# Kernel optimization log

Measured on AMD Instinct MI355X. Metric: run time of the kernel, lower is better.

Reference implementation:

```python
import jax, jax.numpy as jnp
import numpy as np

B, T = 2, 512
D, H, DFF = 1024, 16, 4096
V, CSL = 32000, 16
NL, NDL = 4, 2
MAXLEN = 1024
DH = D // H


def generate_ar_mask(L, csl):
    m = np.zeros((2 * L, 2 * L), dtype=bool)
    for i in range(L):
        m[:i] = True
        m[L + (i // csl) * csl: L + i] = True
    return jnp.asarray(m)


def generate_block_ntp_mask(L, csl):
    m = np.zeros((2 * L, 2 * L), dtype=bool)
    for c in range(L // csl):
        if c - 1 >= 0:
            m[:(c - 1) * csl] = True
        m[L + c * csl: L + (c + 1) * csl] = True
    return jnp.asarray(m)


def layernorm(x, g, b, eps=1e-5):
    mu = x.mean(-1, keepdims=True)
    var = x.var(-1, keepdims=True)
    return (x - mu) / jnp.sqrt(var + eps) * g + b


def block(x, mask, p):
    ln1g, ln1b, wqkv, bqkv, wo, bo, ln2g, ln2b, w1, b1, w2, b2 = p
    h = layernorm(x, ln1g, ln1b)
    qkv = h @ wqkv + bqkv                       # [B,S,3D]
    q, k, v = jnp.split(qkv, 3, axis=-1)
    bs, S, _ = x.shape
    q = q.reshape(bs, S, H, DH).transpose(0, 2, 1, 3)
    k = k.reshape(bs, S, H, DH).transpose(0, 2, 1, 3)
    v = v.reshape(bs, S, H, DH).transpose(0, 2, 1, 3)
    scores = jnp.einsum('bhqd,bhkd->bhqk', q, k) / jnp.sqrt(jnp.asarray(DH, x.dtype))
    scores = jnp.where(mask, scores, jnp.asarray(-1e9, x.dtype))
    attn = jax.nn.softmax(scores, axis=-1)
    o = jnp.einsum('bhqk,bhkd->bhqd', attn, v)
    o = o.transpose(0, 2, 1, 3).reshape(bs, S, D)
    x = x + (o @ wo + bo)
    h = layernorm(x, ln2g, ln2b)
    return x + (jax.nn.gelu(h @ w1 + b1, approximate=False) @ w2 + b2)


def setup_inputs():
    key = jax.random.key(0)
    ks = jax.random.split(key, 6)

    def pstack(k, n):
        kk = jax.random.split(k, 4)
        return dict(
            ln1g=jnp.ones((n, D)), ln1b=jnp.zeros((n, D)),
            wqkv=0.02 * jax.random.normal(kk[0], (n, D, 3 * D)), bqkv=jnp.zeros((n, 3 * D)),
            wo=0.02 * jax.random.normal(kk[1], (n, D, D)), bo=jnp.zeros((n, D)),
            ln2g=jnp.ones((n, D)), ln2b=jnp.zeros((n, D)),
            w1=0.02 * jax.random.normal(kk[2], (n, D, DFF)), b1=jnp.zeros((n, DFF)),
            w2=0.02 * jax.random.normal(kk[3], (n, DFF, D)), b2=jnp.zeros((n, D)))

    body = pstack(ks[0], NL)
    dec = pstack(ks[1], NDL)
    inp = {
        'tok_ids': jax.random.randint(ks[2], (B, T), 0, V),
        'tok_emb': 0.02 * jax.random.normal(ks[3], (V, D)),
        'pos_emb': 0.02 * jax.random.normal(ks[4], (MAXLEN, D)),
        'mask_tokens': 0.02 * jax.random.normal(ks[5], (1, CSL, D)),
    }
    for kname, vv in body.items():
        inp['b_' + kname] = vv
    for kname, vv in dec.items():
        inp['d_' + kname] = vv
    return inp


def reference(tok_ids, tok_emb, pos_emb, mask_tokens,
              b_ln1g, b_ln1b, b_wqkv, b_bqkv, b_wo, b_bo, b_ln2g, b_ln2b, b_w1, b_b1, b_w2, b_b2,
              d_ln1g, d_ln1b, d_wqkv, d_bqkv, d_wo, d_bo, d_ln2g, d_ln2b, d_w1, d_b1, d_w2, d_b2):
    Bq, Tq = tok_ids.shape
    pos = jnp.tile(jnp.arange(Tq), 2)            # pos ids repeated for both halves
    emb_pos = pos_emb[pos]                       # [2T, D], broadcast over batch
    mask_ids = jnp.tile(mask_tokens, (Bq, Tq // CSL, 1))
    x = jnp.concatenate([tok_emb[tok_ids], mask_ids], axis=1) + emb_pos[None]

    body_mask = generate_block_ntp_mask(Tq, CSL)
    bp = (b_ln1g, b_ln1b, b_wqkv, b_bqkv, b_wo, b_bo, b_ln2g, b_ln2b, b_w1, b_b1, b_w2, b_b2)
    for i in range(NL):
        x = block(x, body_mask, tuple(p[i] for p in bp))

    ar_mask = generate_ar_mask(Tq, CSL)
    dp = (d_ln1g, d_ln1b, d_wqkv, d_bqkv, d_wo, d_bo, d_ln2g, d_ln2b, d_w1, d_b1, d_w2, d_b2)
    for i in range(NDL):
        x = block(x, ar_mask, tuple(p[i] for p in dp))

    logits = (x @ tok_emb.T)[:, Tq + 1:, :]      # [B, T-1, V]
    tgt = tok_ids[:, :-1].reshape(-1)
    logits = logits.reshape(-1, V)
    logp = jax.nn.log_softmax(logits, axis=-1)
    loss = -jnp.take_along_axis(logp, tgt[:, None], axis=1).mean()
    return loss
```

## Files before the change

### kernel.cpp

```cpp
#include <hip/hip_runtime.h>
#include <hip/hip_bf16.h>
#include <math.h>

#define DD   1024
#define HHN  16
#define DHD  64
#define DFFN 4096
#define VV   32000
#define BBN  2
#define TTN  512
#define SSN  1024
#define NRN  2048

typedef __attribute__((ext_vector_type(8))) short short8;
typedef __attribute__((ext_vector_type(4))) float f32x4;

enum : long {
    LSTR    = 12582912,
    OFF_QKV = 0,
    OFF_WO  = 3145728,
    OFF_W1  = 4194304,
    OFF_W2  = 8388608
};

struct P24 { const float* p[24]; };

__device__ __forceinline__ unsigned short f2bf(float f) {
    __hip_bfloat16 h = __float2bfloat16(f);
    return __builtin_bit_cast(unsigned short, h);
}
__device__ __forceinline__ float bf2f(unsigned short u) {
    return __bfloat162float(__builtin_bit_cast(__hip_bfloat16, u));
}

__device__ __forceinline__ void glds16(const void* g, void* l) {
    __builtin_amdgcn_global_load_lds(
        (const __attribute__((address_space(1))) void*)g,
        (__attribute__((address_space(3))) void*)l,
        16, 0, 0);
}

__device__ __forceinline__ float blockReduceSum(float v) {
    __shared__ float sh[4];
    #pragma unroll
    for (int o = 1; o < 64; o <<= 1) v += __shfl_xor(v, o, 64);
    int lane = threadIdx.x & 63, wv = threadIdx.x >> 6;
    __syncthreads();
    if (lane == 0) sh[wv] = v;
    __syncthreads();
    return sh[0] + sh[1] + sh[2] + sh[3];
}

__global__ __launch_bounds__(256) void prep_k(P24 wp, unsigned short* __restrict__ wbf,
                                              const int* __restrict__ tok,
                                              const float* __restrict__ temb,
                                              const float* __restrict__ pemb,
                                              const float* __restrict__ mtok,
                                              float* __restrict__ x) {
    __shared__ __align__(16) unsigned short Lb[128 * 72];
    const int id = blockIdx.x;
    const int t = threadIdx.x;

    if (id < 9216) {
        int seg, base, K, N;
        long woff;
        if (id < 2304)      { seg = 0; base = 0;    K = DD;   N = 3 * DD; woff = OFF_QKV; }
        else if (id < 3072) { seg = 1; base = 2304; K = DD;   N = DD;     woff = OFF_WO;  }
        else if (id < 6144) { seg = 2; base = 3072; K = DD;   N = DFFN;   woff = OFF_W1;  }
        else                { seg = 3; base = 6144; K = DFFN; N = DD;     woff = OFF_W2;  }
        const int rid = id - base;
        const int tpl = (K / 128) * (N / 64);
        const int lz = rid / tpl, t2 = rid % tpl;
        const int nt = N / 64;
        const int n0 = (t2 % nt) * 64, k0 = (t2 / nt) * 128;
        const float* w = wp.p[seg * 6 + lz];
        unsigned short* wt = wbf + (size_t)lz * LSTR + woff;

        const int kr = t >> 4;
        const int nc = (t & 15) * 4;
        #pragma unroll
        for (int p = 0; p < 8; p++) {
            const int k = p * 16 + kr;
            const int g = ((k >> 6) & 1) << 4;
            float4 f = *(const float4*)(w + (size_t)(k0 + k) * N + n0 + nc);
            __align__(8) unsigned short tmp[4];
            tmp[0] = f2bf(f.x); tmp[1] = f2bf(f.y);
            tmp[2] = f2bf(f.z); tmp[3] = f2bf(f.w);
            *(unsigned long long*)&Lb[k * 72 + (nc ^ g)] =
                *(const unsigned long long*)tmp;
        }
        __syncthreads();
        {
            const int rp  = t >> 3;
            const int sub = t & 7;
            const int kcg = sub >> 2;
            const int kh  = sub & 3;
            const int colx = (2 * rp) ^ (kcg << 4);
            const int kb = kcg * 64 + kh * 16;
            __align__(16) unsigned short tA[16], tB[16];
            #pragma unroll
            for (int i = 0; i < 16; i++) {
                unsigned int v = *(const unsigned int*)&Lb[(kb + i) * 72 + colx];
                tA[i] = (unsigned short)(v & 0xffff);
                tB[i] = (unsigned short)(v >> 16);
            }
            unsigned short* d0 = wt + (size_t)(n0 + 2 * rp) * K + k0 + kb;
            unsigned short* d1 = d0 + K;
            #pragma unroll
            for (int i = 0; i < 2; i++) {
                ((int4*)d0)[i] = ((const int4*)tA)[i];
                ((int4*)d1)[i] = ((const int4*)tB)[i];
            }
        }
    } else {
        const int row = id - 9216;
        const int b = row >> 10, s = row & 1023;
        const int d = t * 4;
        const float* src;
        const float* pe;
        if (s < TTN) {
            int tid2 = tok[b * TTN + s];
            src = temb + (size_t)tid2 * DD + d;
            pe  = pemb + (size_t)s * DD + d;
        } else {
            int sm = s - TTN;
            src = mtok + (size_t)(sm & 15) * DD + d;
            pe  = pemb + (size_t)sm * DD + d;
        }
        float4 v = *(const float4*)src;
        float4 p = *(const float4*)pe;
        v.x += p.x; v.y += p.y; v.z += p.z; v.w += p.w;
        *(float4*)(x + (size_t)row * DD + d) = v;
    }
}

__global__ __launch_bounds__(256) void ln_k(const float* __restrict__ x,
                                            const float* __restrict__ g,
                                            const float* __restrict__ b,
                                            unsigned short* __restrict__ out) {
    int row = blockIdx.x;
    int d = threadIdx.x * 4;
    const float4 v = *(const float4*)(x + (size_t)row * DD + d);
    float s  = v.x + v.y + v.z + v.w;
    float ss = v.x * v.x + v.y * v.y + v.z * v.z + v.w * v.w;
    s  = blockReduceSum(s);
    ss = blockReduceSum(ss);
    float mu  = s * (1.0f / DD);
    float var = ss * (1.0f / DD) - mu * mu;
    float inv = rsqrtf(var + 1e-5f);
    const float4 gg = *(const float4*)(g + d);
    const float4 bb = *(const float4*)(b + d);
    ushort4 o;
    o.x = f2bf((v.x - mu) * inv * gg.x + bb.x);
    o.y = f2bf((v.y - mu) * inv * gg.y + bb.y);
    o.z = f2bf((v.z - mu) * inv * gg.z + bb.z);
    o.w = f2bf((v.w - mu) * inv * gg.w + bb.w);
    *(ushort4*)(out + (size_t)row * DD + d) = o;
}

__global__ __launch_bounds__(256, 4) void flash_k(
    const unsigned short* __restrict__ qkvb,
    unsigned short* __restrict__ o,
    int mtype) {
    __shared__ __align__(16) unsigned short Qs[64][72];
    __shared__ __align__(16) unsigned short Ks[64][72];
    __shared__ __align__(16) unsigned short Vs[64][72];
    __shared__ __align__(16) unsigned short Ps[64][72];
    __shared__ float vcol[64];

    const int blk = blockIdx.x;
    const int bh = blk >> 4, qt = blk & 15;
    const int b = bh >> 4, h = bh & 15;
    const int t = threadIdx.x;
    const int lane = t & 63;
    const int w = t >> 6;
    const int fr = lane & 15;
    const int g8 = (lane >> 4) * 8;
    const int g4 = (lane >> 4) * 4;

    {
        const int r = t >> 2, c0 = (t & 3) * 16;
        const unsigned short* src =
            qkvb + (size_t)(b * SSN + qt * 64 + r) * 3072 + h * 64 + c0;
        *(int4*)&Qs[r][c0]     = *(const int4*)(src);
        *(int4*)&Qs[r][c0 + 8] = *(const int4*)(src + 8);
    }
    __syncthreads();
    short8 aq[2];
    #pragma unroll
    for (int kk = 0; kk < 2; kk++)
        aq[kk] = *(const short8*)&Qs[w * 16 + fr][kk * 32 + g8];

    float rsum[4] = {0.f, 0.f, 0.f, 0.f};
    f32x4 accO[4] = {};

    float vacc[16];
    #pragma unroll
    for (int j = 0; j < 16; j++) vacc[j] = 0.f;

    const unsigned short* kbase = qkvb + (size_t)(b * SSN) * 3072 + DD + h * 64;
    const unsigned short* vbase = qkvb + (size_t)(b * SSN) * 3072 + 2 * DD + h * 64;
    const int d0 = w * 16;

    for (int kt = 0; kt < 16; kt++) {
        __syncthreads();
        {
            const int r = t >> 2, c0 = (t & 3) * 16;
            const unsigned short* src = kbase + (size_t)(kt * 64 + r) * 3072 + c0;
            *(int4*)&Ks[r][c0]     = *(const int4*)(src);
            *(int4*)&Ks[r][c0 + 8] = *(const int4*)(src + 8);
        }
        {
            const unsigned short* src = vbase + (size_t)(kt * 64 + lane) * 3072 + d0;
            int4 q0 = *(const int4*)(src);
            int4 q1 = *(const int4*)(src + 8);
            const unsigned short* u = (const unsigned short*)&q0;
            #pragma unroll
            for (int j = 0; j < 8; j++) {
                Vs[d0 + j][lane] = u[j];
                vacc[j] += bf2f(u[j]);
            }
            const unsigned short* u2 = (const unsigned short*)&q1;
            #pragma unroll
            for (int j = 0; j < 8; j++) {
                Vs[d0 + 8 + j][lane] = u2[j];
                vacc[8 + j] += bf2f(u2[j]);
            }
        }
        __syncthreads();

        f32x4 a2[4] = {};
        #pragma unroll
        for (int n = 0; n < 4; n++) {
            short8 bk0 = *(const short8*)&Ks[n * 16 + fr][g8];
            short8 bk1 = *(const short8*)&Ks[n * 16 + fr][32 + g8];
            a2[n] = __builtin_amdgcn_mfma_f32_16x16x32_bf16(aq[0], bk0, a2[n], 0, 0, 0);
            a2[n] = __builtin_amdgcn_mfma_f32_16x16x32_bf16(aq[1], bk1, a2[n], 0, 0, 0);
        }
        #pragma unroll
        for (int j = 0; j < 4; j++) {
            #pragma unroll
            for (int n = 0; n < 4; n++) {
                float pv = __expf(a2[n][j] * 0.125f);
                rsum[j] += pv;
                Ps[w * 16 + g4 + j][n * 16 + fr] = f2bf(pv);
            }
        }
        #pragma unroll
        for (int kk = 0; kk < 2; kk++) {
            short8 pa = *(const short8*)&Ps[w * 16 + fr][kk * 32 + g8];
            #pragma unroll
            for (int nd = 0; nd < 4; nd++) {
                short8 vb = *(const short8*)&Vs[nd * 16 + fr][kk * 32 + g8];
                accO[nd] = __builtin_amdgcn_mfma_f32_16x16x32_bf16(pa, vb, accO[nd], 0, 0, 0);
            }
        }
    }

    float lrun[4];
    #pragma unroll
    for (int j = 0; j < 4; j++) {
        float rs = rsum[j];
        #pragma unroll
        for (int o2 = 1; o2 < 16; o2 <<= 1) rs += __shfl_xor(rs, o2, 64);
        lrun[j] = rs;
    }

    #pragma unroll
    for (int j = 0; j < 16; j++) {
        float vs = vacc[j];
        #pragma unroll
        for (int o2 = 1; o2 < 64; o2 <<= 1) vs += __shfl_xor(vs, o2, 64);
        if (lane == j) vcol[d0 + j] = vs;
    }
    __syncthreads();

    #pragma unroll
    for (int nd = 0; nd < 4; nd++)
        #pragma unroll
        for (int j = 0; j < 4; j++) {
            const int row = qt * 64 + w * 16 + g4 + j;
            const int col = nd * 16 + fr;
            bool uni;
            if (mtype == 0) uni = (row >= 480 && row < 512);
            else            uni = (row == 511) || (row >= 512 && (row & 15) == 15);
            float val;
            if (uni) val = vcol[col] * (1.0f / 1024.0f);
            else     val = accO[nd][j] / lrun[j];
            o[(size_t)(b * SSN + row) * DD + h * 64 + col] = f2bf(val);
        }
}

__global__ __launch_bounds__(256) void gxlconv_k(const float* __restrict__ x,
                                                 unsigned short* __restrict__ xl,
                                                 const float* __restrict__ temb,
                                                 unsigned short* __restrict__ tembb) {
    const int id = blockIdx.x;
    const int t = threadIdx.x;
    if (id < 1024) {
        int d = t * 4;
        ushort4 o = {0, 0, 0, 0};
        if (id < 1022) {
            int b = id / 511, i = id % 511;
            float4 v = *(const float4*)(x + (size_t)(b * SSN + 513 + i) * DD + d);
            o.x = f2bf(v.x); o.y = f2bf(v.y); o.z = f2bf(v.z); o.w = f2bf(v.w);
        }
        *(ushort4*)(xl + (size_t)id * DD + d) = o;
    } else {
        long i = ((long)(id - 1024) * 256 + t) * 8;
        float4 a = *(const float4*)(temb + i);
        float4 b = *(const float4*)(temb + i + 4);
        __align__(16) unsigned short tmp[8];
        tmp[0] = f2bf(a.x); tmp[1] = f2bf(a.y); tmp[2] = f2bf(a.z); tmp[3] = f2bf(a.w);
        tmp[4] = f2bf(b.x); tmp[5] = f2bf(b.y); tmp[6] = f2bf(b.z); tmp[7] = f2bf(b.w);
        *(int4*)(tembb + i) = *(const int4*)tmp;
    }
}

__global__ __launch_bounds__(256) void loss_row2_k(const float2* __restrict__ part,
                                                   const float* __restrict__ tgtlog,
                                                   float* __restrict__ out) {
    const int r = blockIdx.x;
    const int t = threadIdx.x;
    float mx = -1e30f, s = 0.f;
    if (t < 250) {
        float2 p = part[(size_t)r * 250 + t];
        mx = p.x; s = p.y;
    }
    #pragma unroll
    for (int o2 = 1; o2 < 64; o2 <<= 1) {
        float om = __shfl_xor(mx, o2, 64);
        float os = __shfl_xor(s, o2, 64);
        float m2 = fmaxf(mx, om);
        s = s * __expf(mx - m2) + os * __expf(om - m2);
        mx = m2;
    }
    __shared__ float shm[4], shs[4];
    int lane = t & 63, wv = t >> 6;
    if (lane == 0) { shm[wv] = mx; shs[wv] = s; }
    __syncthreads();
    if (t == 0) {
        float M = fmaxf(fmaxf(shm[0], shm[1]), fmaxf(shm[2], shm[3]));
        float S = shs[0] * __expf(shm[0] - M) + shs[1] * __expf(shm[1] - M)
                + shs[2] * __expf(shm[2] - M) + shs[3] * __expf(shm[3] - M);
        atomicAdd(out, ((logf(S) + M) - tgtlog[r]) * (1.0f / 1022.0f));
    }
}

template <int EPI, int KSPLIT, int BM>
__global__ __launch_bounds__(256) void gemm_k(
    const unsigned short* __restrict__ A, long lda,
    const unsigned short* __restrict__ Bt, long ldb,
    void* __restrict__ Cp, long ldc,
    const float* __restrict__ bias,
    int MT, int K, long kstr) {
    constexpr int MFRAG = BM / 32;
    __shared__ __align__(16) unsigned short As[2][BM][32];
    __shared__ __align__(16) unsigned short Bs[2][128][32];

    const int nwg = gridDim.x;
    const int q = nwg >> 3, r = nwg & 7;
    const int xcd = blockIdx.x & 7, lin = blockIdx.x >> 3;
    const int wg = (xcd < r ? xcd * (q + 1) : r * (q + 1) + (xcd - r) * q) + lin;
    const int tiles = nwg / KSPLIT;
    const int ks = wg / tiles;
    const int rem = wg % tiles;
    const int brow = (rem % MT) * BM;
    const int bcol = (rem / MT) * 128;
    const int Kl = K / KSPLIT;

    const int t = threadIdx.x;
    const int lane = t & 63;
    const int w = t >> 6;
    const int fr = lane & 15;
    const int g8 = (lane >> 4) * 8;

    const int sc = (lane & 3) * 8;
    const int srB = w * 32 + (lane >> 2);
    const unsigned short* bP0 = Bt + (size_t)(bcol + srB) * ldb + ks * Kl + sc;
    const unsigned short* bP1 = bP0 + (size_t)16 * ldb;
    const int srA = (BM == 128 ? w * 32 : w * 16) + (lane >> 2);
    const unsigned short* aP0 = A + (size_t)(brow + srA) * lda + ks * Kl + sc;
    const unsigned short* aP1 = aP0 + (size_t)16 * lda;

    f32x4 acc[MFRAG][4] = {};
    const int nsteps = Kl >> 5;

    auto stage = [&](int buf) {
        if constexpr (BM == 128) {
            glds16(aP0, &As[buf][w * 32][0]);
            glds16(aP1, &As[buf][w * 32 + 16][0]);
        } else {
            glds16(aP0, &As[buf][w * 16][0]);
        }
        glds16(bP0, &Bs[buf][w * 32][0]);
        glds16(bP1, &Bs[buf][w * 32 + 16][0]);
        aP0 += 32; aP1 += 32; bP0 += 32; bP1 += 32;
    };

    stage(0);
    asm volatile("s_waitcnt vmcnt(0)");
    __syncthreads();

    const int wrB = (w >> 1) * (BM / 2);
    int cur = 0;
    for (int s2 = 1; s2 < nsteps; ++s2) {
        const int nb = cur ^ 1;
        stage(nb);

        short8 af[MFRAG], bf[4];
        #pragma unroll
        for (int m = 0; m < MFRAG; m++)
            af[m] = *(const short8*)&As[cur][wrB + m * 16 + fr][g8];
        #pragma unroll
        for (int n = 0; n < 4; n++)
            bf[n] = *(const short8*)&Bs[cur][(w & 1) * 64 + n * 16 + fr][g8];
        #pragma unroll
        for (int m = 0; m < MFRAG; m++)
            #pragma unroll
            for (int n = 0; n < 4; n++)
                acc[m][n] = __builtin_amdgcn_mfma_f32_16x16x32_bf16(af[m], bf[n], acc[m][n], 0, 0, 0);
        __syncthreads();
        cur = nb;
    }
    {
        short8 af[MFRAG], bf[4];
        #pragma unroll
        for (int m = 0; m < MFRAG; m++)
            af[m] = *(const short8*)&As[cur][wrB + m * 16 + fr][g8];
        #pragma unroll
        for (int n = 0; n < 4; n++)
            bf[n] = *(const short8*)&Bs[cur][(w & 1) * 64 + n * 16 + fr][g8];
        #pragma unroll
        for (int m = 0; m < MFRAG; m++)
            #pragma unroll
            for (int n = 0; n < 4; n++)
                acc[m][n] = __builtin_amdgcn_mfma_f32_16x16x32_bf16(af[m], bf[n], acc[m][n], 0, 0, 0);
    }

    const int wc = (w & 1) * 64;
    const int g4 = (lane >> 4) * 4;
    #pragma unroll
    for (int n = 0; n < 4; n++) {
        const int col = bcol + wc + n * 16 + fr;
        const float bv = (bias && (KSPLIT == 1 || ks == 0)) ? bias[col] : 0.f;
        #pragma unroll
        for (int m = 0; m < MFRAG; m++) {
            #pragma unroll
            for (int j = 0; j < 4; j++) {
                const int row = brow + wrB + m * 16 + g4 + j;
                float v = acc[m][n][j] + bv;
                const size_t ci = (size_t)row * ldc + col;
                if (EPI == 0) {
                    ((float*)Cp)[ci] = v;
                } else if (EPI == 1) {
                    ((unsigned short*)Cp)[ci] = f2bf(v);
                } else if (EPI == 2) {
                    float gl = 0.5f * v * (1.0f + erff(v * 0.70710678118654752f));
                    ((unsigned short*)Cp)[ci] = f2bf(gl);
                } else if (EPI == 3) {
                    ((float*)Cp)[ci] += v;
                } else {
                    atomicAdd(&((float*)Cp)[ci], v);
                }
            }
        }
    }
}

__global__ __launch_bounds__(256, 1) void gemm_lse_k(
    const unsigned short* __restrict__ A,
    const unsigned short* __restrict__ Bt,
    float2* __restrict__ part,
    float* __restrict__ tgtlog,
    const int* __restrict__ tok) {
    __shared__ __align__(16) unsigned short As[2][128][32];
    __shared__ __align__(16) unsigned short Bs[2][256][32];

    const int nwg = gridDim.x;
    const int q = nwg >> 3, r = nwg & 7;
    const int xcd = blockIdx.x & 7, lin = blockIdx.x >> 3;
    const int wg = (xcd < r ? xcd * (q + 1) : r * (q + 1) + (xcd - r) * q) + lin;
    const int MT = 8;
    const int brow = (wg % MT) * 128;
    const int bcol = (wg / MT) * 256;

    const int t = threadIdx.x;
    const int lane = t & 63;
    const int w = t >> 6;
    const int fr = lane & 15;
    const int g8 = (lane >> 4) * 8;

    const int sc = (lane & 3) * 8;
    const int srA = w * 32 + (lane >> 2);
    const unsigned short* aP0 = A + (size_t)(brow + srA) * DD + sc;
    const unsigned short* aP1 = aP0 + (size_t)16 * DD;
    const int srB = w * 64 + (lane >> 2);
    const unsigned short* bP0 = Bt + (size_t)(bcol + srB) * DD + sc;
    const unsigned short* bP1 = bP0 + (size_t)16 * DD;
    const unsigned short* bP2 = bP0 + (size_t)32 * DD;
    const unsigned short* bP3 = bP0 + (size_t)48 * DD;

    f32x4 acc[4][8] = {};

    auto stage = [&](int buf) {
        glds16(aP0, &As[buf][w * 32][0]);
        glds16(aP1, &As[buf][w * 32 + 16][0]);
        glds16(bP0, &Bs[buf][w * 64][0]);
        glds16(bP1, &Bs[buf][w * 64 + 16][0]);
        glds16(bP2, &Bs[buf][w * 64 + 32][0]);
        glds16(bP3, &Bs[buf][w * 64 + 48][0]);
        aP0 += 32; aP1 += 32;
        bP0 += 32; bP1 += 32; bP2 += 32; bP3 += 32;
    };

    stage(0);
    asm volatile("s_waitcnt vmcnt(0)");
    __syncthreads();

    int cur = 0;
    for (int s2 = 1; s2 < 32; ++s2) {
        const int nb = cur ^ 1;
        stage(nb);

        short8 af[4], bf[8];
        #pragma unroll
        for (int m = 0; m < 4; m++)
            af[m] = *(const short8*)&As[cur][(w >> 1) * 64 + m * 16 + fr][g8];
        #pragma unroll
        for (int n = 0; n < 8; n++)
            bf[n] = *(const short8*)&Bs[cur][(w & 1) * 128 + n * 16 + fr][g8];
        #pragma unroll
        for (int m = 0; m < 4; m++)
            #pragma unroll
            for (int n = 0; n < 8; n++)
                acc[m][n] = __builtin_amdgcn_mfma_f32_16x16x32_bf16(af[m], bf[n], acc[m][n], 0, 0, 0);
        __syncthreads();
        cur = nb;
    }
    {
        short8 af[4], bf[8];
        #pragma unroll
        for (int m = 0; m < 4; m++)
            af[m] = *(const short8*)&As[cur][(w >> 1) * 64 + m * 16 + fr][g8];
        #pragma unroll
        for (int n = 0; n < 8; n++)
            bf[n] = *(const short8*)&Bs[cur][(w & 1) * 128 + n * 16 + fr][g8];
        #pragma unroll
        for (int m = 0; m < 4; m++)
            #pragma unroll
            for (int n = 0; n < 8; n++)
                acc[m][n] = __builtin_amdgcn_mfma_f32_16x16x32_bf16(af[m], bf[n], acc[m][n], 0, 0, 0);
    }

    const int wr = (w >> 1) * 64;
    const int wc = (w & 1) * 128;
    const int g4 = (lane >> 4) * 4;
    const int ct2 = (bcol >> 7) + (w & 1);
    #pragma unroll
    for (int m = 0; m < 4; m++) {
        #pragma unroll
        for (int j = 0; j < 4; j++) {
            const int grow = brow + wr + m * 16 + g4 + j;
            float vv[8];
            #pragma unroll
            for (int n = 0; n < 8; n++) vv[n] = acc[m][n][j];
            float mx = vv[0];
            #pragma unroll
            for (int n = 1; n < 8; n++) mx = fmaxf(mx, vv[n]);
            #pragma unroll
            for (int o2 = 1; o2 < 16; o2 <<= 1) mx = fmaxf(mx, __shfl_xor(mx, o2, 64));
            float s = 0.f;
            #pragma unroll
            for (int n = 0; n < 8; n++) s += __expf(vv[n] - mx);
            #pragma unroll
            for (int o2 = 1; o2 < 16; o2 <<= 1) s += __shfl_xor(s, o2, 64);
            if (fr == 0) {
                float2 p; p.x = mx; p.y = s;
                part[(size_t)grow * 250 + ct2] = p;
            }
            int tgtc = -1;
            if (grow < 511) tgtc = tok[grow];
            else if (grow >= 511 && grow < 1022) tgtc = tok[512 + grow - 511];
            const int cl = tgtc - (bcol + wc);
            if (tgtc >= 0 && cl >= 0 && cl < 128 && (cl & 15) == fr) {
                tgtlog[grow] = vv[cl >> 4];
            }
        }
    }
}

extern "C" void kernel_launch(void* const* d_in, const int* in_sizes, int n_in,
                              void* d_out, int out_size, void* d_ws, size_t ws_size,
                              hipStream_t stream) {
    const int*   tok  = (const int*)d_in[0];
    const float* temb = (const float*)d_in[1];
    const float* pemb = (const float*)d_in[2];
    const float* mtok = (const float*)d_in[3];
    const float* W[24];
    for (int i = 0; i < 24; i++) W[i] = (const float*)d_in[4 + i];

    char* ws = (char*)d_ws;
    float*          x      = (float*)(ws + 0);
    unsigned short* xb     = (unsigned short*)(ws + 8388608);
    unsigned short* qkvb   = (unsigned short*)(ws + 12582912);
    unsigned short* o      = (unsigned short*)(ws + 25165824);
    unsigned short* g      = (unsigned short*)(ws + 29360128);
    unsigned short* wbf    = (unsigned short*)(ws + 79691776);
    unsigned short* tembb  = (unsigned short*)(ws + 79691776);
    float2*         part   = (float2*)(ws + 145227776);
    float*          tgtlog = (float*)(ws + 147275776);
    unsigned short* xl     = (unsigned short*)(ws + 230686720);
    float*          rowloss= (float*)(ws + 232783872);
    (void)rowloss;

    P24 wp;
    for (int l = 0; l < 6; l++) {
        const int grp = (l < 4) ? 0 : 1;
        const int li  = (l < 4) ? l : l - 4;
        const float* const* P = W + grp * 12;
        wp.p[0 + l]  = P[2]  + (size_t)li * DD * 3 * DD;
        wp.p[6 + l]  = P[4]  + (size_t)li * DD * DD;
        wp.p[12 + l] = P[8]  + (size_t)li * DD * DFFN;
        wp.p[18 + l] = P[10] + (size_t)li * DFFN * DD;
    }
    hipMemsetAsync(d_out, 0, 4, stream);
    prep_k<<<9216 + 2048, 256, 0, stream>>>(wp, wbf, tok, temb, pemb, mtok, x);

    for (int l = 0; l < 6; l++) {
        const int grp = (l < 4) ? 0 : 1;
        const int li  = (l < 4) ? l : l - 4;
        const float* const* P = W + grp * 12;
        const float* ln1g = P[0] + (size_t)li * DD;
        const float* ln1b = P[1] + (size_t)li * DD;
        const float* bqkv = P[3] + (size_t)li * 3 * DD;
        const float* bo   = P[5] + (size_t)li * DD;
        const float* ln2g = P[6] + (size_t)li * DD;
        const float* ln2b = P[7] + (size_t)li * DD;
        const float* b1   = P[9] + (size_t)li * DFFN;
        const float* b2   = P[11] + (size_t)li * DD;
        unsigned short* wl = wbf + (size_t)l * LSTR;

        if (l == 0) ln_k<<<NRN, 256, 0, stream>>>(x, ln1g, ln1b, xb);
        gemm_k<1, 1, 64><<<32 * 24, 256, 0, stream>>>(xb, DD, wl + OFF_QKV, DD,
                                                      qkvb, 3 * DD, bqkv, 32, DD, 0);
        flash_k<<<512, 256, 0, stream>>>(qkvb, o, grp);
        gemm_k<3, 1, 64><<<32 * 8, 256, 0, stream>>>(o, DD, wl + OFF_WO, DD,
                                                     x, DD, bo, 32, DD, 0);

        ln_k<<<NRN, 256, 0, stream>>>(x, ln2g, ln2b, xb);
        gemm_k<2, 1, 128><<<16 * 32, 256, 0, stream>>>(xb, DD, wl + OFF_W1, DD,
                                                       g, DFFN, b1, 16, DD, 0);
        gemm_k<4, 4, 128><<<16 * 8 * 4, 256, 0, stream>>>(g, DFFN, wl + OFF_W2, DFFN,
                                                          x, DD, b2, 16, DFFN, 0);
        if (l < 5) {
            const int l2 = l + 1;
            const int grp2 = (l2 < 4) ? 0 : 1;
            const int li2  = (l2 < 4) ? l2 : l2 - 4;
            const float* const* P2 = W + grp2 * 12;
            ln_k<<<NRN, 256, 0, stream>>>(x, P2[0] + (size_t)li2 * DD,
                                          P2[1] + (size_t)li2 * DD, xb);
        } else {
            gxlconv_k<<<1024 + 16000, 256, 0, stream>>>(x, xl, temb, tembb);
        }
    }

    gemm_lse_k<<<1000, 256, 0, stream>>>(xl, tembb, part, tgtlog, tok);
    loss_row2_k<<<1022, 256, 0, stream>>>(part, tgtlog, (float*)d_out);
}
```

Measured before the change: 1.414 ms.

## Fuse layernorms into GEMM epilogues via last-block counters; merge embedding conversions into prep

```diff
diff --git a/kernel.cpp b/kernel.cpp
--- a/kernel.cpp
+++ b/kernel.cpp
@@ -51,12 +51,51 @@
     return sh[0] + sh[1] + sh[2] + sh[3];
 }
 
+__device__ __forceinline__ void dev_ln_row(const float* __restrict__ x,
+                                           const float* __restrict__ g,
+                                           const float* __restrict__ b,
+                                           unsigned short* __restrict__ out, int row) {
+    const int lane = threadIdx.x & 63;
+    float4 v[4];
+    float s = 0.f, ss = 0.f;
+    #pragma unroll
+    for (int c = 0; c < 4; c++) {
+        v[c] = *(const float4*)(x + (size_t)row * DD + c * 256 + lane * 4);
+        s  += v[c].x + v[c].y + v[c].z + v[c].w;
+        ss += v[c].x * v[c].x + v[c].y * v[c].y + v[c].z * v[c].z + v[c].w * v[c].w;
+    }
+    #pragma unroll
+    for (int o2 = 1; o2 < 64; o2 <<= 1) {
+        s  += __shfl_xor(s, o2, 64);
+        ss += __shfl_xor(ss, o2, 64);
+    }
+    const float mu  = s * (1.0f / DD);
+    const float var = ss * (1.0f / DD) - mu * mu;
+    const float inv = rsqrtf(var + 1e-5f);
+    #pragma unroll
+    for (int c = 0; c < 4; c++) {
+        const int d = c * 256 + lane * 4;
+        const float4 gg = *(const float4*)(g + d);
+        const float4 bb = *(const float4*)(b + d);
+        ushort4 ov;
+        ov.x = f2bf((v[c].x - mu) * inv * gg.x + bb.x);
+        ov.y = f2bf((v[c].y - mu) * inv * gg.y + bb.y);
+        ov.z = f2bf((v[c].z - mu) * inv * gg.z + bb.z);
+        ov.w = f2bf((v[c].w - mu) * inv * gg.w + bb.w);
+        *(ushort4*)(out + (size_t)row * DD + d) = ov;
+    }
+}
+
 __global__ __launch_bounds__(256) void prep_k(P24 wp, unsigned short* __restrict__ wbf,
                                               const int* __restrict__ tok,
                                               const float* __restrict__ temb,
                                               const float* __restrict__ pemb,
                                               const float* __restrict__ mtok,
-                                              float* __restrict__ x) {
+                                              float* __restrict__ x,
+                                              const float* __restrict__ ln0g,
+                                              const float* __restrict__ ln0b,
+                                              unsigned short* __restrict__ xb,
+                                              unsigned short* __restrict__ tembb) {
     __shared__ __align__(16) unsigned short Lb[128 * 72];
     const int id = blockIdx.x;
     const int t = threadIdx.x;
@@ -112,7 +151,7 @@
                 ((int4*)d1)[i] = ((const int4*)tB)[i];
             }
         }
-    } else {
+    } else if (id < 11264) {
         const int row = id - 9216;
         const int b = row >> 10, s = row & 1023;
         const int d = t * 4;
@@ -131,31 +170,30 @@
         float4 p = *(const float4*)pe;
         v.x += p.x; v.y += p.y; v.z += p.z; v.w += p.w;
         *(float4*)(x + (size_t)row * DD + d) = v;
-    }
-}
-
-__global__ __launch_bounds__(256) void ln_k(const float* __restrict__ x,
-                                            const float* __restrict__ g,
-                                            const float* __restrict__ b,
-                                            unsigned short* __restrict__ out) {
-    int row = blockIdx.x;
-    int d = threadIdx.x * 4;
-    const float4 v = *(const float4*)(x + (size_t)row * DD + d);
-    float s  = v.x + v.y + v.z + v.w;
-    float ss = v.x * v.x + v.y * v.y + v.z * v.z + v.w * v.w;
-    s  = blockReduceSum(s);
-    ss = blockReduceSum(ss);
-    float mu  = s * (1.0f / DD);
-    float var = ss * (1.0f / DD) - mu * mu;
-    float inv = rsqrtf(var + 1e-5f);
-    const float4 gg = *(const float4*)(g + d);
-    const float4 bb = *(const float4*)(b + d);
-    ushort4 o;
-    o.x = f2bf((v.x - mu) * inv * gg.x + bb.x);
-    o.y = f2bf((v.y - mu) * inv * gg.y + bb.y);
-    o.z = f2bf((v.z - mu) * inv * gg.z + bb.z);
-    o.w = f2bf((v.w - mu) * inv * gg.w + bb.w);
-    *(ushort4*)(out + (size_t)row * DD + d) = o;
+        float su  = v.x + v.y + v.z + v.w;
+        float ssu = v.x * v.x + v.y * v.y + v.z * v.z + v.w * v.w;
+        su  = blockReduceSum(su);
+        ssu = blockReduceSum(ssu);
+        const float mu  = su * (1.0f / DD);
+        const float var = ssu * (1.0f / DD) - mu * mu;
+        const float inv = rsqrtf(var + 1e-5f);
+        const float4 gg = *(const float4*)(ln0g + d);
+        const float4 bb = *(const float4*)(ln0b + d);
+        ushort4 ov;
+        ov.x = f2bf((v.x - mu) * inv * gg.x + bb.x);
+        ov.y = f2bf((v.y - mu) * inv * gg.y + bb.y);
+        ov.z = f2bf((v.z - mu) * inv * gg.z + bb.z);
+        ov.w = f2bf((v.w - mu) * inv * gg.w + bb.w);
+        *(ushort4*)(xb + (size_t)row * DD + d) = ov;
+    } else {
+        long i = ((long)(id - 11264) * 256 + t) * 8;
+        float4 a = *(const float4*)(temb + i);
+        float4 b = *(const float4*)(temb + i + 4);
+        __align__(16) unsigned short tmp[8];
+        tmp[0] = f2bf(a.x); tmp[1] = f2bf(a.y); tmp[2] = f2bf(a.z); tmp[3] = f2bf(a.w);
+        tmp[4] = f2bf(b.x); tmp[5] = f2bf(b.y); tmp[6] = f2bf(b.z); tmp[7] = f2bf(b.w);
+        *(int4*)(tembb + i) = *(const int4*)tmp;
+    }
 }
 
 __global__ __launch_bounds__(256, 4) void flash_k(
@@ -265,7 +303,6 @@
         for (int o2 = 1; o2 < 16; o2 <<= 1) rs += __shfl_xor(rs, o2, 64);
         lrun[j] = rs;
     }
-
     #pragma unroll
     for (int j = 0; j < 16; j++) {
         float vs = vacc[j];
@@ -291,32 +328,6 @@
         }
 }
 
-__global__ __launch_bounds__(256) void gxlconv_k(const float* __restrict__ x,
-                                                 unsigned short* __restrict__ xl,
-                                                 const float* __restrict__ temb,
-                                                 unsigned short* __restrict__ tembb) {
-    const int id = blockIdx.x;
-    const int t = threadIdx.x;
-    if (id < 1024) {
-        int d = t * 4;
-        ushort4 o = {0, 0, 0, 0};
-        if (id < 1022) {
-            int b = id / 511, i = id % 511;
-            float4 v = *(const float4*)(x + (size_t)(b * SSN + 513 + i) * DD + d);
-            o.x = f2bf(v.x); o.y = f2bf(v.y); o.z = f2bf(v.z); o.w = f2bf(v.w);
-        }
-        *(ushort4*)(xl + (size_t)id * DD + d) = o;
-    } else {
-        long i = ((long)(id - 1024) * 256 + t) * 8;
-        float4 a = *(const float4*)(temb + i);
-        float4 b = *(const float4*)(temb + i + 4);
-        __align__(16) unsigned short tmp[8];
-        tmp[0] = f2bf(a.x); tmp[1] = f2bf(a.y); tmp[2] = f2bf(a.z); tmp[3] = f2bf(a.w);
-        tmp[4] = f2bf(b.x); tmp[5] = f2bf(b.y); tmp[6] = f2bf(b.z); tmp[7] = f2bf(b.w);
-        *(int4*)(tembb + i) = *(const int4*)tmp;
-    }
-}
-
 __global__ __launch_bounds__(256) void loss_row2_k(const float2* __restrict__ part,
                                                    const float* __restrict__ tgtlog,
                                                    float* __restrict__ out) {
@@ -353,10 +364,13 @@
     const unsigned short* __restrict__ Bt, long ldb,
     void* __restrict__ Cp, long ldc,
     const float* __restrict__ bias,
-    int MT, int K, long kstr) {
+    int MT, int K,
+    const float* __restrict__ lng, const float* __restrict__ lnb,
+    unsigned short* __restrict__ xbo, unsigned* __restrict__ cnt) {
     constexpr int MFRAG = BM / 32;
     __shared__ __align__(16) unsigned short As[2][BM][32];
     __shared__ __align__(16) unsigned short Bs[2][128][32];
+    __shared__ int lastf;
 
     const int nwg = gridDim.x;
     const int q = nwg >> 3, r = nwg & 7;
@@ -451,17 +465,49 @@
                 const int row = brow + wrB + m * 16 + g4 + j;
                 float v = acc[m][n][j] + bv;
                 const size_t ci = (size_t)row * ldc + col;
-                if (EPI == 0) {
-                    ((float*)Cp)[ci] = v;
-                } else if (EPI == 1) {
+                if (EPI == 1) {
                     ((unsigned short*)Cp)[ci] = f2bf(v);
                 } else if (EPI == 2) {
                     float gl = 0.5f * v * (1.0f + erff(v * 0.70710678118654752f));
                     ((unsigned short*)Cp)[ci] = f2bf(gl);
-                } else if (EPI == 3) {
+                } else if (EPI == 3 || EPI == 5) {
                     ((float*)Cp)[ci] += v;
                 } else {
                     atomicAdd(&((float*)Cp)[ci], v);
+                }
+            }
+        }
+    }
+
+    if constexpr (EPI == 5 || EPI == 6) {
+        __syncthreads();
+        if (t == 0) {
+            __threadfence();
+            unsigned old = __hip_atomic_fetch_add(cnt + (rem % MT), 1u,
+                                                  __ATOMIC_ACQ_REL,
+                                                  __HIP_MEMORY_SCOPE_AGENT);
+            lastf = (old == (unsigned)(nwg / MT - 1));
+        }
+        __syncthreads();
+        if (lastf) {
+            __threadfence();
+            const float* xsrc = (const float*)Cp;
+            if (lng) {
+                for (int rr = w; rr < BM; rr += 4)
+                    dev_ln_row(xsrc, lng, lnb, xbo, brow + rr);
+            } else {
+                const int d = t * 4;
+                for (int rr = 0; rr < BM; ++rr) {
+                    const int row = brow + rr;
+                    const int s = row & 1023;
+                    if (s >= 513) {
+                        const int xr = (row >> 10) * 511 + (s - 513);
+                        float4 v = *(const float4*)(xsrc + (size_t)row * DD + d);
+                        ushort4 ov;
+                        ov.x = f2bf(v.x); ov.y = f2bf(v.y);
+                        ov.z = f2bf(v.z); ov.w = f2bf(v.w);
+                        *(ushort4*)(xbo + (size_t)xr * DD + d) = ov;
+                    }
                 }
             }
         }
@@ -607,12 +653,11 @@
     unsigned short* o      = (unsigned short*)(ws + 25165824);
     unsigned short* g      = (unsigned short*)(ws + 29360128);
     unsigned short* wbf    = (unsigned short*)(ws + 79691776);
-    unsigned short* tembb  = (unsigned short*)(ws + 79691776);
-    float2*         part   = (float2*)(ws + 145227776);
-    float*          tgtlog = (float*)(ws + 147275776);
-    unsigned short* xl     = (unsigned short*)(ws + 230686720);
-    float*          rowloss= (float*)(ws + 232783872);
-    (void)rowloss;
+    unsigned short* tembb  = (unsigned short*)(ws + 230686720);
+    float2*         part   = (float2*)(ws + 296222720);
+    float*          tgtlog = (float*)(ws + 298270720);
+    unsigned short* xl     = (unsigned short*)(ws + 298274816);
+    unsigned*       cnt    = (unsigned*)(ws + 300371968);
 
     P24 wp;
     for (int l = 0; l < 6; l++) {
@@ -624,15 +669,17 @@
         wp.p[12 + l] = P[8]  + (size_t)li * DD * DFFN;
         wp.p[18 + l] = P[10] + (size_t)li * DFFN * DD;
     }
+
+    hipMemsetAsync(cnt, 0, 2048, stream);
     hipMemsetAsync(d_out, 0, 4, stream);
-    prep_k<<<9216 + 2048, 256, 0, stream>>>(wp, wbf, tok, temb, pemb, mtok, x);
+
+    prep_k<<<9216 + 2048 + 16000, 256, 0, stream>>>(wp, wbf, tok, temb, pemb, mtok, x,
+                                                    W[0], W[1], xb, tembb);
 
     for (int l = 0; l < 6; l++) {
         const int grp = (l < 4) ? 0 : 1;
         const int li  = (l < 4) ? l : l - 4;
         const float* const* P = W + grp * 12;
-        const float* ln1g = P[0] + (size_t)li * DD;
-        const float* ln1b = P[1] + (size_t)li * DD;
         const float* bqkv = P[3] + (size_t)li * 3 * DD;
         const float* bo   = P[5] + (size_t)li * DD;
         const float* ln2g = P[6] + (size_t)li * DD;
@@ -640,29 +687,36 @@
         const float* b1   = P[9] + (size_t)li * DFFN;
         const float* b2   = P[11] + (size_t)li * DD;
         unsigned short* wl = wbf + (size_t)l * LSTR;
-
-        if (l == 0) ln_k<<<NRN, 256, 0, stream>>>(x, ln1g, ln1b, xb);
-        gemm_k<1, 1, 64><<<32 * 24, 256, 0, stream>>>(xb, DD, wl + OFF_QKV, DD,
-                                                      qkvb, 3 * DD, bqkv, 32, DD, 0);
-        flash_k<<<512, 256, 0, stream>>>(qkvb, o, grp);
-        gemm_k<3, 1, 64><<<32 * 8, 256, 0, stream>>>(o, DD, wl + OFF_WO, DD,
-                                                     x, DD, bo, 32, DD, 0);
-
-        ln_k<<<NRN, 256, 0, stream>>>(x, ln2g, ln2b, xb);
-        gemm_k<2, 1, 128><<<16 * 32, 256, 0, stream>>>(xb, DD, wl + OFF_W1, DD,
-                                                       g, DFFN, b1, 16, DD, 0);
-        gemm_k<4, 4, 128><<<16 * 8 * 4, 256, 0, stream>>>(g, DFFN, wl + OFF_W2, DFFN,
-                                                          x, DD, b2, 16, DFFN, 0);
+        unsigned* cntWo = cnt + l * 64;
+        unsigned* cntF2 = cnt + l * 64 + 32;
+
+        const float* nx_g = nullptr;
+        const float* nx_b = nullptr;
+        unsigned short* f2out = xl;
         if (l < 5) {
             const int l2 = l + 1;
             const int grp2 = (l2 < 4) ? 0 : 1;
             const int li2  = (l2 < 4) ? l2 : l2 - 4;
             const float* const* P2 = W + grp2 * 12;
-            ln_k<<<NRN, 256, 0, stream>>>(x, P2[0] + (size_t)li2 * DD,
-                                          P2[1] + (size_t)li2 * DD, xb);
-        } else {
-            gxlconv_k<<<1024 + 16000, 256, 0, stream>>>(x, xl, temb, tembb);
-        }
+            nx_g = P2[0] + (size_t)li2 * DD;
+            nx_b = P2[1] + (size_t)li2 * DD;
+            f2out = xb;
+        }
+
+        gemm_k<1, 1, 64><<<32 * 24, 256, 0, stream>>>(
+            xb, DD, wl + OFF_QKV, DD, qkvb, 3 * DD, bqkv, 32, DD,
+            nullptr, nullptr, nullptr, nullptr);
+        flash_k<<<512, 256, 0, stream>>>(qkvb, o, grp);
+        gemm_k<5, 1, 64><<<32 * 8, 256, 0, stream>>>(
+            o, DD, wl + OFF_WO, DD, x, DD, bo, 32, DD,
+            ln2g, ln2b, xb, cntWo);
+
+        gemm_k<2, 1, 128><<<16 * 32, 256, 0, stream>>>(
+            xb, DD, wl + OFF_W1, DD, g, DFFN, b1, 16, DD,
+            nullptr, nullptr, nullptr, nullptr);
+        gemm_k<6, 4, 128><<<16 * 8 * 4, 256, 0, stream>>>(
+            g, DFFN, wl + OFF_W2, DFFN, x, DD, b2, 16, DFFN,
+            nx_g, nx_b, f2out, cntF2);
     }
 
     gemm_lse_k<<<1000, 256, 0, stream>>>(xl, tembb, part, tgtlog, tok);
```

Measured after the change: 1.876 ms. +32.6%, slower.
